# Optimization experiments

Measured on AMD Instinct MI355X. Metric: run time of the kernel, lower is better.

The kernel has to match this reference:

```python
import jax, jax.numpy as jnp
import numpy as np
import math

V, D, H, L, DFF = 32000, 1024, 16, 4, 4096
B, T_TGT, T_SRC = 4, 512, 512


def setup_inputs() -> dict:
    key = jax.random.key(0)
    ks = iter(jax.random.split(key, 64))
    s = 0.02
    inp = {
        'tgt': jax.random.randint(next(ks), (B, T_TGT), 0, V, dtype=jnp.int32),
        'encoder_output': jax.random.normal(next(ks), (B, T_SRC, D), jnp.float32),
        'tgt_mask': jnp.tril(jnp.ones((T_TGT, T_TGT), jnp.int32)),
        'emb': jax.random.normal(next(ks), (V, D)) * s,
        'Wout': jax.random.normal(next(ks), (D, V)) * s,
        'bout': jnp.zeros((V,)),
    }
    for pfx in ('s', 'c'):  # self / cross attention
        for nm in ('q', 'k', 'v', 'o'):
            inp[f'W{nm}_{pfx}'] = jax.random.normal(next(ks), (L, D, D)) * s
            inp[f'b{nm}_{pfx}'] = jnp.zeros((L, D))
    inp['W1'] = jax.random.normal(next(ks), (L, D, DFF)) * s
    inp['b1'] = jnp.zeros((L, DFF))
    inp['W2'] = jax.random.normal(next(ks), (L, DFF, D)) * s
    inp['b2'] = jnp.zeros((L, D))
    for i in (1, 2, 3):
        inp[f'ln{i}_g'] = jnp.ones((L, D))
        inp[f'ln{i}_b'] = jnp.zeros((L, D))
    return inp


def _layernorm(x, g, b, eps=1e-5):
    m = x.mean(-1, keepdims=True)
    v = ((x - m) ** 2).mean(-1, keepdims=True)
    return g * (x - m) * jax.lax.rsqrt(v + eps) + b


def _mha(xq, xkv, Wq, bq, Wk, bk, Wv, bv, Wo, bo, mask):
    Bq, Tq, Dm = xq.shape
    dk = Dm // H
    q = (xq @ Wq + bq).reshape(Bq, Tq, H, dk).transpose(0, 2, 1, 3)   # bhqd
    k = (xkv @ Wk + bk).reshape(Bq, -1, H, dk).transpose(0, 2, 1, 3)  # bhkd
    v = (xkv @ Wv + bv).reshape(Bq, -1, H, dk).transpose(0, 2, 1, 3)
    scores = jnp.einsum('bhqd,bhkd->bhqk', q, k) / math.sqrt(dk)
    if mask is not None:
        scores = jnp.where(mask[None, None] == 0, -1e9, scores)
    w = jax.nn.softmax(scores, axis=-1)                               # dropout: eval mode
    o = jnp.einsum('bhqk,bhkd->bhqd', w, v).transpose(0, 2, 1, 3).reshape(Bq, Tq, Dm)
    return o @ Wo + bo, w


def _pos_encoding(T, Dm):
    pos = jnp.arange(T, dtype=jnp.float32)[:, None]
    div = jnp.exp(jnp.arange(0, Dm, 2, dtype=jnp.float32) * (-math.log(10000.0) / Dm))
    pe = jnp.zeros((T, Dm))
    pe = pe.at[:, 0::2].set(jnp.sin(pos * div))
    pe = pe.at[:, 1::2].set(jnp.cos(pos * div))
    return pe


def reference(tgt, encoder_output, tgt_mask, emb, Wout, bout,
              Wq_s, bq_s, Wk_s, bk_s, Wv_s, bv_s, Wo_s, bo_s,
              Wq_c, bq_c, Wk_c, bk_c, Wv_c, bv_c, Wo_c, bo_c,
              W1, b1, W2, b2, ln1_g, ln1_b, ln2_g, ln2_b, ln3_g, ln3_b):
    x = emb[tgt] * math.sqrt(D) + _pos_encoding(tgt.shape[1], D)[None]
    self_ws, cross_ws = [], []
    for i in range(L):
        a1, sw = _mha(x, x, Wq_s[i], bq_s[i], Wk_s[i], bk_s[i], Wv_s[i], bv_s[i],
                      Wo_s[i], bo_s[i], tgt_mask)
        x = _layernorm(x + a1, ln1_g[i], ln1_b[i])
        a2, cw = _mha(x, encoder_output, Wq_c[i], bq_c[i], Wk_c[i], bk_c[i],
                      Wv_c[i], bv_c[i], Wo_c[i], bo_c[i], None)
        x = _layernorm(x + a2, ln2_g[i], ln2_b[i])
        ffn = jax.nn.relu(x @ W1[i] + b1[i]) @ W2[i] + b2[i]
        x = _layernorm(x + ffn, ln3_g[i], ln3_b[i])
        self_ws.append(sw)
        cross_ws.append(cw)
    logits = x @ Wout + bout
    return logits, jnp.stack(self_ws), jnp.stack(cross_ws)
```

## Files before the change

### kernel.cpp

```cpp
#include <hip/hip_runtime.h>


typedef unsigned short u16;
typedef __bf16 v8bf __attribute__((ext_vector_type(8)));
typedef float v4f __attribute__((ext_vector_type(4)));

namespace {
constexpr int kB = 4, kT = 512, kD = 1024, kH = 16, kDK = 64, kF = 4096, kV = 32000, kL = 4;
constexpr int kM = kB * kT;
constexpr long kTD = (long)kT * kD;
constexpr long kTT = (long)kT * kT;
constexpr long kHTT = (long)kH * kTT;
constexpr long kBHTT = (long)kB * kHTT;
constexpr long kLOG = (long)kM * kV;
constexpr long kPART = (long)kM * kD;
}

__device__ __forceinline__ u16 f2bf(float f) {
  union { float f; unsigned u; } v; v.f = f;
  unsigned r = v.u + 0x7FFFu + ((v.u >> 16) & 1u);
  return (u16)(r >> 16);
}
__device__ __forceinline__ float bf2f(u16 h) {
  union { unsigned u; float f; } v; v.u = ((unsigned)h) << 16;
  return v.f;
}

typedef __attribute__((address_space(3))) void lds_void;
typedef const __attribute__((address_space(1))) void glob_void;
__device__ __forceinline__ void gl2lds16(const void* g, void* l) {
  __builtin_amdgcn_global_load_lds((glob_void*)g, (lds_void*)l, 16, 0, 0);
}

template <int BM, int BN, int OUTBF>
__global__ __launch_bounds__(256)
void gemm_bf(const u16* __restrict__ A0, const u16* __restrict__ B0,
             const float* __restrict__ bias, void* __restrict__ Cv,
             const int K, const int lda, const int ldb, const int ldc,
             const int nH, const long sAb, const long sAh,
             const long sBb, const long sBh, const long sCb, const long sCh,
             const float scale, const int relu) {
  static_assert(BM % 32 == 0 && BN % 32 == 0, "tiles");
  __shared__ u16 As[BM][64];
  __shared__ u16 Bs[BN][64];
  const int tid = threadIdx.x;
  const int lane = tid & 63;
  const int w = tid >> 6;
  const int z = blockIdx.z;
  const int zb = z / nH, zh = z - zb * nH;
  const u16* A = A0 + zb * sAb + zh * sAh + (long)blockIdx.y * BM * lda;
  const u16* B = B0 + zb * sBb + zh * sBh + (long)blockIdx.x * BN * ldb;
  const long offC = zb * sCb + zh * sCh;
  const int wm = w >> 1, wn = w & 1;
  constexpr int FM = BM / 32, FN = BN / 32;
  v4f acc[FM][FN];
  const v4f zero = {0.f, 0.f, 0.f, 0.f};
#pragma unroll
  for (int i = 0; i < FM; ++i)
#pragma unroll
    for (int j = 0; j < FN; ++j) acc[i][j] = zero;
  const int l15 = lane & 15, lk = lane >> 4;
  const int lr8 = lane >> 3;
  const int lc8 = (lane & 7) * 8;

  for (int k0 = 0; k0 < K; k0 += 64) {
    __syncthreads();
#pragma unroll
    for (int s = 0; s < BM / 32; ++s)
      gl2lds16(A + (long)(w * (BM / 4) + s * 8 + lr8) * lda + k0 + lc8,
               &As[w * (BM / 4) + s * 8][0]);
#pragma unroll
    for (int s = 0; s < BN / 32; ++s)
      gl2lds16(B + (long)(w * (BN / 4) + s * 8 + lr8) * ldb + k0 + lc8,
               &Bs[w * (BN / 4) + s * 8][0]);
    __syncthreads();
#pragma unroll
    for (int t = 0; t < 2; ++t) {
      v8bf af[FM], bfr[FN];
#pragma unroll
      for (int i = 0; i < FM; ++i)
        af[i] = *(const v8bf*)&As[wm * (BM / 2) + i * 16 + l15][t * 32 + lk * 8];
#pragma unroll
      for (int j = 0; j < FN; ++j)
        bfr[j] = *(const v8bf*)&Bs[wn * (BN / 2) + j * 16 + l15][t * 32 + lk * 8];
#pragma unroll
      for (int i = 0; i < FM; ++i)
#pragma unroll
        for (int j = 0; j < FN; ++j)
          acc[i][j] = __builtin_amdgcn_mfma_f32_16x16x32_bf16(af[i], bfr[j], acc[i][j], 0, 0, 0);
    }
  }

  const long m0 = (long)blockIdx.y * BM + wm * (BM / 2);
  const int n0 = blockIdx.x * BN + wn * (BN / 2);
#pragma unroll
  for (int j = 0; j < FN; ++j) {
    const int col = n0 + j * 16 + l15;
    const float bv = (bias && zb == 0) ? bias[col] : 0.0f;
#pragma unroll
    for (int i = 0; i < FM; ++i) {
      const long row = m0 + i * 16 + lk * 4;
#pragma unroll
      for (int r = 0; r < 4; ++r) {
        float v = acc[i][j][r] * scale + bv;
        if (relu) v = fmaxf(v, 0.0f);
        const long idx = offC + (row + r) * ldc + col;
        if (OUTBF) ((u16*)Cv)[idx] = f2bf(v);
        else       ((float*)Cv)[idx] = v;
      }
    }
  }
}

template <int CAUSAL>
__global__ __launch_bounds__(512)
void attn_scores(const u16* __restrict__ Qb, const u16* __restrict__ Kb,
                 float* __restrict__ wout, u16* __restrict__ pb) {
  __shared__ u16 Qs[128][64];
  __shared__ u16 Ks[512][64];
  __shared__ float redM[128][4];
  __shared__ float redS[128][4];
  const int tid = threadIdx.x, lane = tid & 63, w = tid >> 6;
  const int wm = w >> 2, wn = w & 3;
  const int l15 = lane & 15, lk = lane >> 4;
  const int lr8 = lane >> 3, lc8 = (lane & 7) * 8;
  const int bx = blockIdx.x;
  const int z = blockIdx.y, zb = z >> 4, zh = z & 15;
  const u16* Q = Qb + (long)zb * 512 * 3072 + zh * 64 + (long)bx * 128 * 3072;
  const u16* Kp = Kb + (long)zb * 512 * 3072 + zh * 64;
  const long obase = (long)zb * kHTT + (long)zh * kTT;

#pragma unroll
  for (int s = 0; s < 2; ++s)
    gl2lds16(Q + (long)(w * 16 + s * 8 + lr8) * 3072 + lc8, &Qs[w * 16 + s * 8][0]);
#pragma unroll
  for (int s = 0; s < 8; ++s) {
    const int r0 = w * 64 + s * 8;
    if (!CAUSAL || r0 <= bx * 128 + 127)
      gl2lds16(Kp + (long)(r0 + lr8) * 3072 + lc8, &Ks[r0][0]);
  }
  __syncthreads();

  v4f acc[4][8];
  const v4f zero = {0.f, 0.f, 0.f, 0.f};
#pragma unroll
  for (int i = 0; i < 4; ++i)
#pragma unroll
    for (int j = 0; j < 8; ++j) acc[i][j] = zero;

#pragma unroll
  for (int t = 0; t < 2; ++t) {
    v8bf aq[4], bk[8];
#pragma unroll
    for (int i = 0; i < 4; ++i)
      aq[i] = *(const v8bf*)&Qs[wm * 64 + i * 16 + l15][t * 32 + lk * 8];
#pragma unroll
    for (int j = 0; j < 8; ++j)
      bk[j] = *(const v8bf*)&Ks[wn * 128 + j * 16 + l15][t * 32 + lk * 8];
#pragma unroll
    for (int i = 0; i < 4; ++i)
#pragma unroll
      for (int j = 0; j < 8; ++j) {
        if (!(CAUSAL && wn * 128 + j * 16 > bx * 128 + wm * 64 + i * 16 + 15))
          acc[i][j] = __builtin_amdgcn_mfma_f32_16x16x32_bf16(aq[i], bk[j], acc[i][j], 0, 0, 0);
      }
  }

  float gmax[4][4];
#pragma unroll
  for (int i = 0; i < 4; ++i)
#pragma unroll
    for (int r = 0; r < 4; ++r) {
      const int q = bx * 128 + wm * 64 + i * 16 + lk * 4 + r;
      float m = -3.0e38f;
#pragma unroll
      for (int j = 0; j < 8; ++j) {
        const int col = wn * 128 + j * 16 + l15;
        if (!CAUSAL || col <= q) m = fmaxf(m, acc[i][j][r] * 0.125f);
      }
#pragma unroll
      for (int off = 1; off < 16; off <<= 1) m = fmaxf(m, __shfl_xor(m, off));
      if (l15 == 0) redM[wm * 64 + i * 16 + lk * 4 + r][wn] = m;
    }
  __syncthreads();
#pragma unroll
  for (int i = 0; i < 4; ++i)
#pragma unroll
    for (int r = 0; r < 4; ++r) {
      v4f mv = *(const v4f*)&redM[wm * 64 + i * 16 + lk * 4 + r][0];
      gmax[i][r] = fmaxf(fmaxf(mv[0], mv[1]), fmaxf(mv[2], mv[3]));
    }
#pragma unroll
  for (int i = 0; i < 4; ++i)
#pragma unroll
    for (int r = 0; r < 4; ++r) {
      const int q = bx * 128 + wm * 64 + i * 16 + lk * 4 + r;
      float s = 0.0f;
#pragma unroll
      for (int j = 0; j < 8; ++j) {
        const int col = wn * 128 + j * 16 + l15;
        float e = (!CAUSAL || col <= q) ? __expf(acc[i][j][r] * 0.125f - gmax[i][r]) : 0.0f;
        acc[i][j][r] = e;
        s += e;
      }
#pragma unroll
      for (int off = 1; off < 16; off <<= 1) s += __shfl_xor(s, off);
      if (l15 == 0) redS[wm * 64 + i * 16 + lk * 4 + r][wn] = s;
    }
  __syncthreads();
#pragma unroll
  for (int i = 0; i < 4; ++i)
#pragma unroll
    for (int r = 0; r < 4; ++r) {
      v4f sv = *(const v4f*)&redS[wm * 64 + i * 16 + lk * 4 + r][0];
      const float inv = 1.0f / (sv[0] + sv[1] + sv[2] + sv[3]);
      const int q = bx * 128 + wm * 64 + i * 16 + lk * 4 + r;
      const long rowoff = obase + (long)q * 512;
#pragma unroll
      for (int j = 0; j < 8; ++j) {
        const int col = wn * 128 + j * 16 + l15;
        const float v = acc[i][j][r] * inv;
        wout[rowoff + col] = v;
        pb[rowoff + col] = f2bf(v);
      }
    }
}

struct TPtrs { const float* in[8]; u16* out[8]; };

__global__ void transpose_wt_v2(TPtrs ps, int K, int N) {
  __shared__ float tile[32][33];
  const float* in = ps.in[blockIdx.z];
  u16* o = ps.out[blockIdx.z];
  const int n0 = blockIdx.x * 32, k0 = blockIdx.y * 32;
  const int tx = threadIdx.x, ty = threadIdx.y;
#pragma unroll
  for (int i = 0; i < 4; ++i)
    tile[ty + 8 * i][tx] = in[(long)(k0 + ty + 8 * i) * N + n0 + tx];
  __syncthreads();
#pragma unroll
  for (int i = 0; i < 4; ++i)
    o[(long)(n0 + ty + 8 * i) * K + k0 + tx] = f2bf(tile[tx][ty + 8 * i]);
}

__global__ void concat_bias(float* __restrict__ dst, const float* __restrict__ s0,
                            const float* __restrict__ s1, const float* __restrict__ s2,
                            const int nsrc) {
  const int idx = blockIdx.x * 256 + threadIdx.x;
  const int per = nsrc << 10;
  const int l = idx / per, rem = idx - l * per, s = rem >> 10, j = rem & 1023;
  const float* src = (s == 0) ? s0 : (s == 1 ? s1 : s2);
  dst[idx] = src[l * 1024 + j];
}

__global__ void cvt_bf16_v2(const float* __restrict__ in, u16* __restrict__ o) {
  const long i = ((long)blockIdx.x * 256 + threadIdx.x) * 4;
  float4 v = *(const float4*)(in + i);
  u16 h[4] = {f2bf(v.x), f2bf(v.y), f2bf(v.z), f2bf(v.w)};
  *(uint2*)(o + i) = *(const uint2*)h;
}

__global__ void embed_v2(const int* __restrict__ tgt, const float* __restrict__ emb,
                         float* __restrict__ x, u16* __restrict__ xb) {
  const int row = blockIdx.x;
  const int t = row & (kT - 1);
  const int tok = tgt[row];
  const int c = threadIdx.x * 4;
  float4 e = *(const float4*)(emb + (long)tok * kD + c);
  const float nl = -9.210340371976184f / (float)kD;
  const float a0 = (float)t * expf((float)c * nl);
  const float a1 = (float)t * expf((float)(c + 2) * nl);
  float4 o;
  o.x = e.x * 32.0f + sinf(a0);
  o.y = e.y * 32.0f + cosf(a0);
  o.z = e.z * 32.0f + sinf(a1);
  o.w = e.w * 32.0f + cosf(a1);
  *(float4*)(x + (long)row * kD + c) = o;
  u16 h[4] = {f2bf(o.x), f2bf(o.y), f2bf(o.z), f2bf(o.w)};
  *(uint2*)(xb + (long)row * kD + c) = *(const uint2*)h;
}

__global__ void transpose_v_v2(const u16* __restrict__ Sqkv, u16* __restrict__ vt) {
  __shared__ u16 tile[32][33];
  const int z = blockIdx.z, b = z >> 4, h = z & 15;
  const int t0 = blockIdx.x * 32, d0 = blockIdx.y * 32;
  const int tx = threadIdx.x, ty = threadIdx.y;
  const u16* in = Sqkv + (long)b * kT * 3072 + 2048 + h * kDK;
#pragma unroll
  for (int i = 0; i < 4; ++i)
    tile[ty + 8 * i][tx] = in[(long)(t0 + ty + 8 * i) * 3072 + d0 + tx];
  __syncthreads();
  u16* o = vt + (long)z * kDK * kT;
#pragma unroll
  for (int i = 0; i < 4; ++i)
    o[(long)(d0 + ty + 8 * i) * kT + t0 + tx] = tile[tx][ty + 8 * i];
}

__global__ void add_ln_v3(float* __restrict__ x, u16* __restrict__ xb,
                          const float* __restrict__ res, const int nres,
                          const float* __restrict__ g, const float* __restrict__ b) {
  const int row = blockIdx.x;
  const int c = threadIdx.x * 4;
  float4 xv = *(const float4*)(x + (long)row * kD + c);
  float v0 = xv.x, v1 = xv.y, v2 = xv.z, v3 = xv.w;
  for (int p = 0; p < nres; ++p) {
    float4 rv = *(const float4*)(res + p * kPART + (long)row * kD + c);
    v0 += rv.x; v1 += rv.y; v2 += rv.z; v3 += rv.w;
  }
  float s = v0 + v1 + v2 + v3;
  float ss = v0 * v0 + v1 * v1 + v2 * v2 + v3 * v3;
#pragma unroll
  for (int o = 32; o > 0; o >>= 1) { s += __shfl_xor(s, o); ss += __shfl_xor(ss, o); }
  __shared__ float red[4][2];
  const int wv = threadIdx.x >> 6;
  if ((threadIdx.x & 63) == 0) { red[wv][0] = s; red[wv][1] = ss; }
  __syncthreads();
  s  = red[0][0] + red[1][0] + red[2][0] + red[3][0];
  ss = red[0][1] + red[1][1] + red[2][1] + red[3][1];
  const float mean = s * (1.0f / kD);
  const float var = ss * (1.0f / kD) - mean * mean;
  const float rs = rsqrtf(var + 1e-5f);
  float4 gv = *(const float4*)(g + c);
  float4 bv = *(const float4*)(b + c);
  float4 o;
  o.x = gv.x * (v0 - mean) * rs + bv.x;
  o.y = gv.y * (v1 - mean) * rs + bv.y;
  o.z = gv.z * (v2 - mean) * rs + bv.z;
  o.w = gv.w * (v3 - mean) * rs + bv.w;
  *(float4*)(x + (long)row * kD + c) = o;
  u16 h[4] = {f2bf(o.x), f2bf(o.y), f2bf(o.z), f2bf(o.w)};
  *(uint2*)(xb + (long)row * kD + c) = *(const uint2*)h;
}

template <int BM, int BN, typename TA, typename TB, int BKN>
__global__ __launch_bounds__(256)
void gemm_kernel(const void* __restrict__ Av, const void* __restrict__ Bv,
                 const float* __restrict__ bias, float* __restrict__ Cv,
                 const int K, const int lda, const int ldb, const int ldc,
                 const int nH, const long sAb, const long sAh,
                 const long sBb, const long sBh, const long sCb, const long sCh,
                 const float scale, const int relu) {
  constexpr int LP = 40;
  __shared__ u16 As[BM][LP];
  __shared__ u16 Bs[BN][LP];
  const int tid = threadIdx.x;
  const int z = blockIdx.z;
  const int zb = z / nH, zh = z - zb * nH;
  const TA* A = (const TA*)Av + zb * sAb + zh * sAh + (long)blockIdx.y * BM * lda;
  const TB* Bp;
  if constexpr (BKN)
    Bp = (const TB*)Bv + zb * sBb + zh * sBh + (long)blockIdx.x * BN;
  else
    Bp = (const TB*)Bv + zb * sBb + zh * sBh + (long)blockIdx.x * BN * ldb;
  const long offC = zb * sCb + zh * sCh;
  const int lane = tid & 63;
  const int wm = (tid >> 7) & 1, wn = (tid >> 6) & 1;
  constexpr int FM = BM / 32, FN = BN / 32;
  v4f acc[FM][FN];
  const v4f zero = {0.f, 0.f, 0.f, 0.f};
#pragma unroll
  for (int i = 0; i < FM; ++i)
#pragma unroll
    for (int j = 0; j < FN; ++j) acc[i][j] = zero;
  const int l15 = lane & 15, lk = lane >> 4;

  for (int k0 = 0; k0 < K; k0 += 32) {
    __syncthreads();
    if constexpr (sizeof(TA) == 4) {
      const int r = tid >> 3, c = (tid & 7) * 4;
#pragma unroll
      for (int rr = 0; rr < BM; rr += 32) {
        float4 vv = *(const float4*)((const float*)A + (long)(rr + r) * lda + k0 + c);
        unsigned lo = (unsigned)f2bf(vv.x) | ((unsigned)f2bf(vv.y) << 16);
        unsigned hi = (unsigned)f2bf(vv.z) | ((unsigned)f2bf(vv.w) << 16);
        *(uint2*)&As[rr + r][c] = make_uint2(lo, hi);
      }
    } else {
      const int r = tid >> 2, c = (tid & 3) * 8;
#pragma unroll
      for (int rr = 0; rr < BM; rr += 64) {
        uint4 vv = *(const uint4*)((const u16*)A + (long)(rr + r) * lda + k0 + c);
        *(uint4*)&As[rr + r][c] = vv;
      }
    }
    if constexpr (BKN) {
      const int r = tid >> 3, c = (tid & 7) * 4;
#pragma unroll
      for (int nn = 0; nn < BN; nn += 32) {
        float4 vv = *(const float4*)((const float*)Bp + (long)(k0 + r) * ldb + nn + c);
        Bs[nn + c + 0][r] = f2bf(vv.x);
        Bs[nn + c + 1][r] = f2bf(vv.y);
        Bs[nn + c + 2][r] = f2bf(vv.z);
        Bs[nn + c + 3][r] = f2bf(vv.w);
      }
    } else if constexpr (sizeof(TB) == 4) {
      const int r = tid >> 3, c = (tid & 7) * 4;
#pragma unroll
      for (int rr = 0; rr < BN; rr += 32) {
        float4 vv = *(const float4*)((const float*)Bp + (long)(rr + r) * ldb + k0 + c);
        unsigned lo = (unsigned)f2bf(vv.x) | ((unsigned)f2bf(vv.y) << 16);
        unsigned hi = (unsigned)f2bf(vv.z) | ((unsigned)f2bf(vv.w) << 16);
        *(uint2*)&Bs[rr + r][c] = make_uint2(lo, hi);
      }
    } else {
      const int r = tid >> 2, c = (tid & 3) * 8;
#pragma unroll
      for (int rr = 0; rr < BN; rr += 64) {
        uint4 vv = *(const uint4*)((const u16*)Bp + (long)(rr + r) * ldb + k0 + c);
        *(uint4*)&Bs[rr + r][c] = vv;
      }
    }
    __syncthreads();
    v8bf af[FM], bfr[FN];
#pragma unroll
    for (int i = 0; i < FM; ++i)
      af[i] = *(const v8bf*)&As[wm * (BM / 2) + i * 16 + l15][lk * 8];
#pragma unroll
    for (int j = 0; j < FN; ++j)
      bfr[j] = *(const v8bf*)&Bs[wn * (BN / 2) + j * 16 + l15][lk * 8];
#pragma unroll
    for (int i = 0; i < FM; ++i)
#pragma unroll
      for (int j = 0; j < FN; ++j)
        acc[i][j] = __builtin_amdgcn_mfma_f32_16x16x32_bf16(af[i], bfr[j], acc[i][j], 0, 0, 0);
  }

  const long m0 = (long)blockIdx.y * BM + wm * (BM / 2);
  const int n0 = blockIdx.x * BN + wn * (BN / 2);
#pragma unroll
  for (int j = 0; j < FN; ++j) {
    const int col = n0 + j * 16 + l15;
    const float bv = bias ? bias[col] : 0.0f;
#pragma unroll
    for (int i = 0; i < FM; ++i) {
      const long row = m0 + i * 16 + lk * 4;
#pragma unroll
      for (int r = 0; r < 4; ++r) {
        float v = acc[i][j][r] * scale + bv;
        if (relu) v = fmaxf(v, 0.0f);
        Cv[offC + (row + r) * ldc + col] = v;
      }
    }
  }
}

__global__ void embed_kernel(const int* __restrict__ tgt, const float* __restrict__ emb,
                             float* __restrict__ x) {
  const int row = blockIdx.x;
  const int t = row & (kT - 1);
  const int tok = tgt[row];
  const int c = threadIdx.x * 4;
  float4 e = *(const float4*)(emb + (long)tok * kD + c);
  const float nl = -9.210340371976184f / (float)kD;
  const float a0 = (float)t * expf((float)c * nl);
  const float a1 = (float)t * expf((float)(c + 2) * nl);
  float4 o;
  o.x = e.x * 32.0f + sinf(a0);
  o.y = e.y * 32.0f + cosf(a0);
  o.z = e.z * 32.0f + sinf(a1);
  o.w = e.w * 32.0f + cosf(a1);
  *(float4*)(x + (long)row * kD + c) = o;
}

__global__ void transpose_v_kernel(const float* __restrict__ v, u16* __restrict__ vt) {
  __shared__ float tile[32][33];
  const int z = blockIdx.z;
  const int b = z >> 4, h = z & 15;
  const int t0 = blockIdx.x * 32, d0 = blockIdx.y * 32;
  const int tx = threadIdx.x, ty = threadIdx.y;
  const float* in = v + (long)b * kTD + (long)h * kDK;
#pragma unroll
  for (int i = 0; i < 4; ++i)
    tile[ty + 8 * i][tx] = in[(long)(t0 + ty + 8 * i) * kD + d0 + tx];
  __syncthreads();
  u16* o = vt + (long)z * kDK * kT;
#pragma unroll
  for (int i = 0; i < 4; ++i)
    o[(long)(d0 + ty + 8 * i) * kT + t0 + tx] = f2bf(tile[tx][ty + 8 * i]);
}

__global__ void softmax_kernel(float* __restrict__ w, const int causal) {
  const int rowg = blockIdx.x * 4 + (threadIdx.x >> 6);
  const int lane = threadIdx.x & 63;
  const int q = rowg & (kT - 1);
  float* p = w + (long)rowg * kT + lane * 8;
  float4 v0 = *(const float4*)p;
  float4 v1 = *(const float4*)(p + 4);
  float f[8] = {v0.x, v0.y, v0.z, v0.w, v1.x, v1.y, v1.z, v1.w};
  const int base = lane * 8;
  float mx = -3.0e38f;
#pragma unroll
  for (int j = 0; j < 8; ++j)
    if (!causal || base + j <= q) mx = fmaxf(mx, f[j]);
#pragma unroll
  for (int o = 32; o > 0; o >>= 1) mx = fmaxf(mx, __shfl_xor(mx, o));
  float s = 0.0f;
#pragma unroll
  for (int j = 0; j < 8; ++j) {
    float e = (!causal || base + j <= q) ? __expf(f[j] - mx) : 0.0f;
    f[j] = e; s += e;
  }
#pragma unroll
  for (int o = 32; o > 0; o >>= 1) s += __shfl_xor(s, o);
  const float inv = 1.0f / s;
  float4 o0 = {f[0] * inv, f[1] * inv, f[2] * inv, f[3] * inv};
  float4 o1 = {f[4] * inv, f[5] * inv, f[6] * inv, f[7] * inv};
  *(float4*)p = o0;
  *(float4*)(p + 4) = o1;
}

__global__ void add_ln_kernel(float* __restrict__ x, const float* __restrict__ res,
                              const float* __restrict__ g, const float* __restrict__ b) {
  const int row = blockIdx.x;
  const int c = threadIdx.x * 4;
  float4 xv = *(const float4*)(x + (long)row * kD + c);
  float4 rv = *(const float4*)(res + (long)row * kD + c);
  const float v0 = xv.x + rv.x, v1 = xv.y + rv.y, v2 = xv.z + rv.z, v3 = xv.w + rv.w;
  float s = v0 + v1 + v2 + v3;
  float ss = v0 * v0 + v1 * v1 + v2 * v2 + v3 * v3;
#pragma unroll
  for (int o = 32; o > 0; o >>= 1) { s += __shfl_xor(s, o); ss += __shfl_xor(ss, o); }
  __shared__ float red[4][2];
  const int wv = threadIdx.x >> 6;
  if ((threadIdx.x & 63) == 0) { red[wv][0] = s; red[wv][1] = ss; }
  __syncthreads();
  s  = red[0][0] + red[1][0] + red[2][0] + red[3][0];
  ss = red[0][1] + red[1][1] + red[2][1] + red[3][1];
  const float mean = s * (1.0f / kD);
  const float var = ss * (1.0f / kD) - mean * mean;
  const float rs = rsqrtf(var + 1e-5f);
  float4 gv = *(const float4*)(g + c);
  float4 bv = *(const float4*)(b + c);
  float4 o;
  o.x = gv.x * (v0 - mean) * rs + bv.x;
  o.y = gv.y * (v1 - mean) * rs + bv.y;
  o.z = gv.z * (v2 - mean) * rs + bv.z;
  o.w = gv.w * (v3 - mean) * rs + bv.w;
  *(float4*)(x + (long)row * kD + c) = o;
}

extern "C" void kernel_launch(void* const* d_in, const int* in_sizes, int n_in,
                              void* d_out, int out_size, void* d_ws, size_t ws_size,
                              hipStream_t stream) {
  const int*   tgt  = (const int*)d_in[0];
  const float* enc  = (const float*)d_in[1];
  const float* emb  = (const float*)d_in[3];
  const float* Wout = (const float*)d_in[4];
  const float* bout = (const float*)d_in[5];
  const float* Wq_s = (const float*)d_in[6];
  const float* bq_s = (const float*)d_in[7];
  const float* Wk_s = (const float*)d_in[8];
  const float* bk_s = (const float*)d_in[9];
  const float* Wv_s = (const float*)d_in[10];
  const float* bv_s = (const float*)d_in[11];
  const float* Wo_s = (const float*)d_in[12];
  const float* bo_s = (const float*)d_in[13];
  const float* Wq_c = (const float*)d_in[14];
  const float* bq_c = (const float*)d_in[15];
  const float* Wk_c = (const float*)d_in[16];
  const float* bk_c = (const float*)d_in[17];
  const float* Wv_c = (const float*)d_in[18];
  const float* bv_c = (const float*)d_in[19];
  const float* Wo_c = (const float*)d_in[20];
  const float* bo_c = (const float*)d_in[21];
  const float* W1   = (const float*)d_in[22];
  const float* b1   = (const float*)d_in[23];
  const float* W2   = (const float*)d_in[24];
  const float* b2   = (const float*)d_in[25];
  const float* ln1g = (const float*)d_in[26];
  const float* ln1b = (const float*)d_in[27];
  const float* ln2g = (const float*)d_in[28];
  const float* ln2b = (const float*)d_in[29];
  const float* ln3g = (const float*)d_in[30];
  const float* ln3b = (const float*)d_in[31];

  float* out = (float*)d_out;
  const long DD = (long)kD * kD;
  const dim3 blk256(256), blkT(32, 8);

  if (ws_size >= (320ll << 20)) {
    char* ws = (char*)d_ws;
    float* x     = (float*)ws;
    u16* xb      = (u16*)(ws + (8l << 20));
    u16* encb    = (u16*)(ws + (12l << 20));
    u16* Sqkv    = (u16*)(ws + (16l << 20));
    u16* vt      = (u16*)(ws + (28l << 20));
    u16* S3b     = (u16*)(ws + (32l << 20));
    u16* Hb      = (u16*)(ws + (36l << 20));
    float* Spart = (float*)(ws + (52l << 20));
    u16* Pb      = (u16*)(ws + (84l << 20));
    u16* wbase   = (u16*)(ws + (116l << 20));
    u16* woutT   = (u16*)(ws + (244l << 20));
    float* bqkvS = (float*)(ws + (308l << 20));
    float* bkvC  = (float*)(ws + (308l << 20) + (64l << 10));
    const long WLAY = (32l << 20) / 2;

    for (int i = 0; i < kL; ++i) {
      u16* wqkvS = wbase + i * WLAY;
      u16* woS   = wqkvS + 3072 * 1024;
      u16* wqC   = woS + 1024 * 1024;
      u16* wkvC  = wqC + 1024 * 1024;
      u16* woC   = wkvC + 2048 * 1024;
      u16* w1t   = woC + 1024 * 1024;
      u16* w2t   = w1t + (long)4096 * 1024;
      TPtrs p{};
      p.in[0] = Wq_s + i * DD; p.out[0] = wqkvS;
      p.in[1] = Wk_s + i * DD; p.out[1] = wqkvS + 1024 * 1024;
      p.in[2] = Wv_s + i * DD; p.out[2] = wqkvS + 2048 * 1024;
      p.in[3] = Wo_s + i * DD; p.out[3] = woS;
      p.in[4] = Wq_c + i * DD; p.out[4] = wqC;
      p.in[5] = Wk_c + i * DD; p.out[5] = wkvC;
      p.in[6] = Wv_c + i * DD; p.out[6] = wkvC + 1024 * 1024;
      p.in[7] = Wo_c + i * DD; p.out[7] = woC;
      transpose_wt_v2<<<dim3(32, 32, 8), blkT, 0, stream>>>(p, 1024, 1024);
      TPtrs p1{}; p1.in[0] = W1 + (long)i * kD * kF; p1.out[0] = w1t;
      transpose_wt_v2<<<dim3(128, 32, 1), blkT, 0, stream>>>(p1, 1024, 4096);
      TPtrs p2{}; p2.in[0] = W2 + (long)i * kF * kD; p2.out[0] = w2t;
      transpose_wt_v2<<<dim3(32, 128, 1), blkT, 0, stream>>>(p2, 4096, 1024);
    }
    TPtrs po{}; po.in[0] = Wout; po.out[0] = woutT;
    transpose_wt_v2<<<dim3(1000, 32, 1), blkT, 0, stream>>>(po, 1024, 32000);
    concat_bias<<<dim3(48), blk256, 0, stream>>>(bqkvS, bq_s, bk_s, bv_s, 3);
    concat_bias<<<dim3(32), blk256, 0, stream>>>(bkvC, bk_c, bv_c, nullptr, 2);
    cvt_bf16_v2<<<dim3(2048), blk256, 0, stream>>>(enc, encb);
    embed_v2<<<dim3(kM), blk256, 0, stream>>>(tgt, emb, x, xb);

    for (int i = 0; i < kL; ++i) {
      u16* wqkvS = wbase + i * WLAY;
      u16* woS   = wqkvS + 3072 * 1024;
      u16* wqC   = woS + 1024 * 1024;
      u16* wkvC  = wqC + 1024 * 1024;
      u16* woC   = wkvC + 2048 * 1024;
      u16* w1t   = woC + 1024 * 1024;
      u16* w2t   = w1t + (long)4096 * 1024;
      float* wSelf  = out + kLOG + (long)i * kBHTT;
      float* wCross = out + kLOG + (long)kL * kBHTT + (long)i * kBHTT;

      gemm_bf<128, 128, 1><<<dim3(24, 16, 1), blk256, 0, stream>>>(
          xb, wqkvS, bqkvS + i * 3072, Sqkv, 1024, 1024, 1024, 3072,
          1, 0, 0, 0, 0, 0, 0, 1.0f, 0);
      transpose_v_v2<<<dim3(16, 2, 64), blkT, 0, stream>>>(Sqkv, vt);
      attn_scores<1><<<dim3(4, 64), dim3(512), 0, stream>>>(Sqkv, Sqkv + 1024, wSelf, Pb);
      gemm_bf<128, 64, 1><<<dim3(1, 4, 64), blk256, 0, stream>>>(
          Pb, vt, nullptr, S3b, 512, 512, 512, 1024,
          16, kHTT, kTT, 16l * 32768, 32768, 512l * 1024, 64, 1.0f, 0);
      gemm_bf<128, 128, 0><<<dim3(8, 16, 2), blk256, 0, stream>>>(
          S3b, woS, bo_s + (long)i * kD, Spart, 512, 1024, 1024, 1024,
          1, 512, 0, 512, 0, kPART, 0, 1.0f, 0);
      add_ln_v3<<<dim3(kM), blk256, 0, stream>>>(x, xb, Spart, 2,
          ln1g + (long)i * kD, ln1b + (long)i * kD);

      gemm_bf<128, 128, 1><<<dim3(8, 16, 1), blk256, 0, stream>>>(
          xb, wqC, bq_c + (long)i * kD, Sqkv, 1024, 1024, 1024, 3072,
          1, 0, 0, 0, 0, 0, 0, 1.0f, 0);
      gemm_bf<128, 128, 1><<<dim3(16, 16, 1), blk256, 0, stream>>>(
          encb, wkvC, bkvC + i * 2048, Sqkv + 1024, 1024, 1024, 1024, 3072,
          1, 0, 0, 0, 0, 0, 0, 1.0f, 0);
      transpose_v_v2<<<dim3(16, 2, 64), blkT, 0, stream>>>(Sqkv, vt);
      attn_scores<0><<<dim3(4, 64), dim3(512), 0, stream>>>(Sqkv, Sqkv + 1024, wCross, Pb);
      gemm_bf<128, 64, 1><<<dim3(1, 4, 64), blk256, 0, stream>>>(
          Pb, vt, nullptr, S3b, 512, 512, 512, 1024,
          16, kHTT, kTT, 16l * 32768, 32768, 512l * 1024, 64, 1.0f, 0);
      gemm_bf<128, 128, 0><<<dim3(8, 16, 2), blk256, 0, stream>>>(
          S3b, woC, bo_c + (long)i * kD, Spart, 512, 1024, 1024, 1024,
          1, 512, 0, 512, 0, kPART, 0, 1.0f, 0);
      add_ln_v3<<<dim3(kM), blk256, 0, stream>>>(x, xb, Spart, 2,
          ln2g + (long)i * kD, ln2b + (long)i * kD);

      gemm_bf<128, 128, 1><<<dim3(32, 16, 1), blk256, 0, stream>>>(
          xb, w1t, b1 + (long)i * kF, Hb, 1024, 1024, 1024, 4096,
          1, 0, 0, 0, 0, 0, 0, 1.0f, 1);
      gemm_bf<128, 128, 0><<<dim3(8, 16, 4), blk256, 0, stream>>>(
          Hb, w2t, b2 + (long)i * kD, Spart, 1024, 4096, 4096, 1024,
          1, 1024, 0, 1024, 0, kPART, 0, 1.0f, 0);
      add_ln_v3<<<dim3(kM), blk256, 0, stream>>>(x, xb, Spart, 4,
          ln3g + (long)i * kD, ln3b + (long)i * kD);
    }

    gemm_bf<128, 128, 0><<<dim3(250, 16, 1), blk256, 0, stream>>>(
        xb, woutT, bout, out, 1024, 1024, 1024, 32000,
        1, 0, 0, 0, 0, 0, 0, 1.0f, 0);
    return;
  }

  float* x = (float*)d_ws;
  char* sc = (char*)d_out;
  float* S0 = (float*)sc;
  float* S1 = (float*)(sc + (8l  << 20));
  float* S2 = (float*)(sc + (16l << 20));
  float* S3 = (float*)(sc + (24l << 20));
  float* S4 = (float*)(sc + (32l << 20));
  u16*   vt = (u16*)  (sc + (40l << 20));

  embed_kernel<<<dim3(kM), blk256, 0, stream>>>(tgt, emb, x);
  auto wgemm = [&](const float* A, const float* W, const float* bias, float* C) {
    gemm_kernel<128, 128, float, float, 1><<<dim3(kD / 128, kM / 128, 1), blk256, 0, stream>>>(
        A, W, bias, C, kD, kD, kD, kD, 1, 0, 0, 0, 0, 0, 0, 1.0f, 0);
  };
  for (int i = 0; i < kL; ++i) {
    const long wOff = (long)i * DD;
    float* wSelf  = out + kLOG + (long)i * kBHTT;
    float* wCross = out + kLOG + (long)kL * kBHTT + (long)i * kBHTT;
    wgemm(x, Wq_s + wOff, bq_s + (long)i * kD, S0);
    wgemm(x, Wk_s + wOff, bk_s + (long)i * kD, S1);
    wgemm(x, Wv_s + wOff, bv_s + (long)i * kD, S2);
    transpose_v_kernel<<<dim3(16, 2, 64), blkT, 0, stream>>>(S2, vt);
    gemm_kernel<128, 128, float, float, 0><<<dim3(4, 4, 64), blk256, 0, stream>>>(
        S0, S1, nullptr, wSelf, kDK, kD, kD, kT,
        kH, kTD, (long)kDK, kTD, (long)kDK, kHTT, kTT, 0.125f, 0);
    softmax_kernel<<<dim3(kB * kH * kT / 4), blk256, 0, stream>>>(wSelf, 1);
    gemm_kernel<128, 64, float, u16, 0><<<dim3(1, 4, 64), blk256, 0, stream>>>(
        wSelf, vt, nullptr, S3, kT, kT, kT, kD,
        kH, kHTT, kTT, (long)kH * kDK * kT, (long)kDK * kT, kTD, (long)kDK, 1.0f, 0);
    wgemm(S3, Wo_s + wOff, bo_s + (long)i * kD, S0);
    add_ln_kernel<<<dim3(kM), blk256, 0, stream>>>(x, S0, ln1g + (long)i * kD, ln1b + (long)i * kD);
    wgemm(x,   Wq_c + wOff, bq_c + (long)i * kD, S0);
    wgemm(enc, Wk_c + wOff, bk_c + (long)i * kD, S1);
    wgemm(enc, Wv_c + wOff, bv_c + (long)i * kD, S2);
    transpose_v_kernel<<<dim3(16, 2, 64), blkT, 0, stream>>>(S2, vt);
    gemm_kernel<128, 128, float, float, 0><<<dim3(4, 4, 64), blk256, 0, stream>>>(
        S0, S1, nullptr, wCross, kDK, kD, kD, kT,
        kH, kTD, (long)kDK, kTD, (long)kDK, kHTT, kTT, 0.125f, 0);
    softmax_kernel<<<dim3(kB * kH * kT / 4), blk256, 0, stream>>>(wCross, 0);
    gemm_kernel<128, 64, float, u16, 0><<<dim3(1, 4, 64), blk256, 0, stream>>>(
        wCross, vt, nullptr, S3, kT, kT, kT, kD,
        kH, kHTT, kTT, (long)kH * kDK * kT, (long)kDK * kT, kTD, (long)kDK, 1.0f, 0);
    wgemm(S3, Wo_c + wOff, bo_c + (long)i * kD, S0);
    add_ln_kernel<<<dim3(kM), blk256, 0, stream>>>(x, S0, ln2g + (long)i * kD, ln2b + (long)i * kD);
    gemm_kernel<128, 128, float, float, 1><<<dim3(kF / 128, kM / 128, 1), blk256, 0, stream>>>(
        x, W1 + (long)i * kD * kF, b1 + (long)i * kF, S0, kD, kD, kF, kF,
        1, 0, 0, 0, 0, 0, 0, 1.0f, 1);
    gemm_kernel<128, 128, float, float, 1><<<dim3(kD / 128, kM / 128, 1), blk256, 0, stream>>>(
        S0, W2 + (long)i * kF * kD, b2 + (long)i * kD, S4, kF, kF, kD, kD,
        1, 0, 0, 0, 0, 0, 0, 1.0f, 0);
    add_ln_kernel<<<dim3(kM), blk256, 0, stream>>>(x, S4, ln3g + (long)i * kD, ln3b + (long)i * kD);
  }
  gemm_kernel<128, 128, float, float, 1><<<dim3(kV / 128, kM / 128, 1), blk256, 0, stream>>>(
      x, Wout, bout, out, kD, kD, kV, kV,
      1, 0, 0, 0, 0, 0, 0, 1.0f, 0);
}
```

Before: 1.685 ms.

## Fuse attention PV into score kernel, swizzle LDS, merge cross-attn QKV GEMMs

Attention now computes P·V inside the softmax kernel, using LDS staging, instead of writing a bf16 probability matrix and running a separate batched GEMM. The V-transpose kernel is removed: the QKV GEMM epilogue writes transposed V directly. LDS tiles in the GEMM and attention kernels use an XOR swizzle to reduce bank conflicts. Cross-attention Q and KV projections are merged into one launch via the z dimension, and FFN2 split-K drops from 4 to 2 partials. In exchange, the epilogue does extra scattered stores and the fused kernel loops serially over key chunks.

```diff
diff --git a/kernel.cpp b/kernel.cpp
--- a/kernel.cpp
+++ b/kernel.cpp
@@ -32,14 +32,15 @@
   __builtin_amdgcn_global_load_lds((glob_void*)g, (lds_void*)l, 16, 0, 0);
 }
 
-template <int BM, int BN, int OUTBF>
+template <int BM, int BN, int OUTBF, int VTR>
 __global__ __launch_bounds__(256)
 void gemm_bf(const u16* __restrict__ A0, const u16* __restrict__ B0,
              const float* __restrict__ bias, void* __restrict__ Cv,
+             u16* __restrict__ vtw,
              const int K, const int lda, const int ldb, const int ldc,
              const int nH, const long sAb, const long sAh,
              const long sBb, const long sBh, const long sCb, const long sCh,
-             const float scale, const int relu) {
+             const float scale, const int relu, const int bstride) {
   static_assert(BM % 32 == 0 && BN % 32 == 0, "tiles");
   __shared__ u16 As[BM][64];
   __shared__ u16 Bs[BN][64];
@@ -61,28 +62,30 @@
     for (int j = 0; j < FN; ++j) acc[i][j] = zero;
   const int l15 = lane & 15, lk = lane >> 4;
   const int lr8 = lane >> 3;
-  const int lc8 = (lane & 7) * 8;
+  const int swz = ((lane & 7) ^ lr8) * 8;
+  const int l7 = l15 & 7;
 
   for (int k0 = 0; k0 < K; k0 += 64) {
     __syncthreads();
 #pragma unroll
     for (int s = 0; s < BM / 32; ++s)
-      gl2lds16(A + (long)(w * (BM / 4) + s * 8 + lr8) * lda + k0 + lc8,
+      gl2lds16(A + (long)(w * (BM / 4) + s * 8 + lr8) * lda + k0 + swz,
                &As[w * (BM / 4) + s * 8][0]);
 #pragma unroll
     for (int s = 0; s < BN / 32; ++s)
-      gl2lds16(B + (long)(w * (BN / 4) + s * 8 + lr8) * ldb + k0 + lc8,
+      gl2lds16(B + (long)(w * (BN / 4) + s * 8 + lr8) * ldb + k0 + swz,
                &Bs[w * (BN / 4) + s * 8][0]);
     __syncthreads();
 #pragma unroll
     for (int t = 0; t < 2; ++t) {
+      const int c0 = t * 4;
       v8bf af[FM], bfr[FN];
 #pragma unroll
       for (int i = 0; i < FM; ++i)
-        af[i] = *(const v8bf*)&As[wm * (BM / 2) + i * 16 + l15][t * 32 + lk * 8];
+        af[i] = *(const v8bf*)&As[wm * (BM / 2) + i * 16 + l15][((c0 + lk) ^ l7) * 8];
 #pragma unroll
       for (int j = 0; j < FN; ++j)
-        bfr[j] = *(const v8bf*)&Bs[wn * (BN / 2) + j * 16 + l15][t * 32 + lk * 8];
+        bfr[j] = *(const v8bf*)&Bs[wn * (BN / 2) + j * 16 + l15][((c0 + lk) ^ l7) * 8];
 #pragma unroll
       for (int i = 0; i < FM; ++i)
 #pragma unroll
@@ -96,7 +99,7 @@
 #pragma unroll
   for (int j = 0; j < FN; ++j) {
     const int col = n0 + j * 16 + l15;
-    const float bv = (bias && zb == 0) ? bias[col] : 0.0f;
+    const float bv = (bias && zb == 0) ? bias[zh * bstride + col] : 0.0f;
 #pragma unroll
     for (int i = 0; i < FM; ++i) {
       const long row = m0 + i * 16 + lk * 4;
@@ -107,6 +110,14 @@
         const long idx = offC + (row + r) * ldc + col;
         if (OUTBF) ((u16*)Cv)[idx] = f2bf(v);
         else       ((float*)Cv)[idx] = v;
+        if (VTR) {
+          const int colS = (int)(offC % 3072) + col;
+          if (colS >= 2048) {
+            const int hh = (colS - 2048) >> 6, dd = (colS - 2048) & 63;
+            const int rowg = (int)(row + r);
+            vtw[((long)((rowg >> 9) * 16 + hh)) * 32768 + dd * 512 + (rowg & 511)] = f2bf(v);
+          }
+        }
       }
     }
   }
@@ -114,30 +125,37 @@
 
 template <int CAUSAL>
 __global__ __launch_bounds__(512)
-void attn_scores(const u16* __restrict__ Qb, const u16* __restrict__ Kb,
-                 float* __restrict__ wout, u16* __restrict__ pb) {
-  __shared__ u16 Qs[128][64];
-  __shared__ u16 Ks[512][64];
+void attn_fused(const u16* __restrict__ Qb, const u16* __restrict__ Kb,
+                const u16* __restrict__ vtp, float* __restrict__ wout,
+                u16* __restrict__ oout) {
+  __shared__ __align__(16) char lds[81920];
+  u16 (*Qs)[64] = (u16 (*)[64])lds;
+  u16 (*Ks)[64] = (u16 (*)[64])(lds + 16384);
+  u16 (*Pl)[136] = (u16 (*)[136])lds;
+  u16 (*Vt)[136] = (u16 (*)[136])(lds + 34816);
   __shared__ float redM[128][4];
   __shared__ float redS[128][4];
   const int tid = threadIdx.x, lane = tid & 63, w = tid >> 6;
   const int wm = w >> 2, wn = w & 3;
   const int l15 = lane & 15, lk = lane >> 4;
-  const int lr8 = lane >> 3, lc8 = (lane & 7) * 8;
+  const int lr8 = lane >> 3;
+  const int swz = ((lane & 7) ^ lr8) * 8;
+  const int l7 = l15 & 7;
   const int bx = blockIdx.x;
   const int z = blockIdx.y, zb = z >> 4, zh = z & 15;
   const u16* Q = Qb + (long)zb * 512 * 3072 + zh * 64 + (long)bx * 128 * 3072;
   const u16* Kp = Kb + (long)zb * 512 * 3072 + zh * 64;
+  const u16* vtz = vtp + (long)((zb << 4) + zh) * 32768;
   const long obase = (long)zb * kHTT + (long)zh * kTT;
 
 #pragma unroll
   for (int s = 0; s < 2; ++s)
-    gl2lds16(Q + (long)(w * 16 + s * 8 + lr8) * 3072 + lc8, &Qs[w * 16 + s * 8][0]);
+    gl2lds16(Q + (long)(w * 16 + s * 8 + lr8) * 3072 + swz, &Qs[w * 16 + s * 8][0]);
 #pragma unroll
   for (int s = 0; s < 8; ++s) {
     const int r0 = w * 64 + s * 8;
     if (!CAUSAL || r0 <= bx * 128 + 127)
-      gl2lds16(Kp + (long)(r0 + lr8) * 3072 + lc8, &Ks[r0][0]);
+      gl2lds16(Kp + (long)(r0 + lr8) * 3072 + swz, &Ks[r0][0]);
   }
   __syncthreads();
 
@@ -150,20 +168,20 @@
 
 #pragma unroll
   for (int t = 0; t < 2; ++t) {
+    const int c0 = t * 4;
     v8bf aq[4], bk[8];
 #pragma unroll
     for (int i = 0; i < 4; ++i)
-      aq[i] = *(const v8bf*)&Qs[wm * 64 + i * 16 + l15][t * 32 + lk * 8];
+      aq[i] = *(const v8bf*)&Qs[wm * 64 + i * 16 + l15][((c0 + lk) ^ l7) * 8];
 #pragma unroll
     for (int j = 0; j < 8; ++j)
-      bk[j] = *(const v8bf*)&Ks[wn * 128 + j * 16 + l15][t * 32 + lk * 8];
+      bk[j] = *(const v8bf*)&Ks[wn * 128 + j * 16 + l15][((c0 + lk) ^ l7) * 8];
 #pragma unroll
     for (int i = 0; i < 4; ++i)
 #pragma unroll
-      for (int j = 0; j < 8; ++j) {
+      for (int j = 0; j < 8; ++j)
         if (!(CAUSAL && wn * 128 + j * 16 > bx * 128 + wm * 64 + i * 16 + 15))
           acc[i][j] = __builtin_amdgcn_mfma_f32_16x16x32_bf16(aq[i], bk[j], acc[i][j], 0, 0, 0);
-      }
   }
 
   float gmax[4][4];
@@ -220,9 +238,52 @@
       for (int j = 0; j < 8; ++j) {
         const int col = wn * 128 + j * 16 + l15;
         const float v = acc[i][j][r] * inv;
+        acc[i][j][r] = v;
         wout[rowoff + col] = v;
-        pb[rowoff + col] = f2bf(v);
-      }
+      }
+    }
+
+  v4f acco[4];
+#pragma unroll
+  for (int i = 0; i < 4; ++i) acco[i] = zero;
+  const int kcMax = CAUSAL ? bx : 3;
+  for (int kc = 0; kc <= kcMax; ++kc) {
+    __syncthreads();
+    if (wn == kc) {
+#pragma unroll
+      for (int i = 0; i < 4; ++i)
+#pragma unroll
+        for (int j = 0; j < 8; ++j) {
+          const int colk = j * 16 + l15;
+#pragma unroll
+          for (int r = 0; r < 4; ++r)
+            Pl[wm * 64 + i * 16 + lk * 4 + r][colk] = f2bf(acc[i][j][r]);
+        }
+    }
+#pragma unroll
+    for (int s = 0; s < 2; ++s) {
+      const int c = tid * 2 + s;
+      const int d = c >> 4, off = (c & 15) * 8;
+      uint4 vv = *(const uint4*)(vtz + (long)d * 512 + kc * 128 + off);
+      *(uint4*)&Vt[d][off] = vv;
+    }
+    __syncthreads();
+#pragma unroll
+    for (int t = 0; t < 4; ++t) {
+      v8bf bv = *(const v8bf*)&Vt[wn * 16 + l15][t * 32 + lk * 8];
+#pragma unroll
+      for (int i = 0; i < 4; ++i) {
+        v8bf ap = *(const v8bf*)&Pl[wm * 64 + i * 16 + l15][t * 32 + lk * 8];
+        acco[i] = __builtin_amdgcn_mfma_f32_16x16x32_bf16(ap, bv, acco[i], 0, 0, 0);
+      }
+    }
+  }
+#pragma unroll
+  for (int i = 0; i < 4; ++i)
+#pragma unroll
+    for (int r = 0; r < 4; ++r) {
+      const int row = bx * 128 + wm * 64 + i * 16 + lk * 4 + r;
+      oout[(long)(zb * 512 + row) * 1024 + zh * 64 + wn * 16 + l15] = f2bf(acco[i][r]);
     }
 }
 
@@ -253,11 +314,13 @@
   dst[idx] = src[l * 1024 + j];
 }
 
-__global__ void cvt_bf16_v2(const float* __restrict__ in, u16* __restrict__ o) {
+__global__ void cvt_bf16_v3(const float* __restrict__ in, u16* __restrict__ o1,
+                            u16* __restrict__ o2) {
   const long i = ((long)blockIdx.x * 256 + threadIdx.x) * 4;
   float4 v = *(const float4*)(in + i);
   u16 h[4] = {f2bf(v.x), f2bf(v.y), f2bf(v.z), f2bf(v.w)};
-  *(uint2*)(o + i) = *(const uint2*)h;
+  *(uint2*)(o1 + i) = *(const uint2*)h;
+  *(uint2*)(o2 + i) = *(const uint2*)h;
 }
 
 __global__ void embed_v2(const int* __restrict__ tgt, const float* __restrict__ emb,
@@ -278,22 +341,6 @@
   *(float4*)(x + (long)row * kD + c) = o;
   u16 h[4] = {f2bf(o.x), f2bf(o.y), f2bf(o.z), f2bf(o.w)};
   *(uint2*)(xb + (long)row * kD + c) = *(const uint2*)h;
-}
-
-__global__ void transpose_v_v2(const u16* __restrict__ Sqkv, u16* __restrict__ vt) {
-  __shared__ u16 tile[32][33];
-  const int z = blockIdx.z, b = z >> 4, h = z & 15;
-  const int t0 = blockIdx.x * 32, d0 = blockIdx.y * 32;
-  const int tx = threadIdx.x, ty = threadIdx.y;
-  const u16* in = Sqkv + (long)b * kT * 3072 + 2048 + h * kDK;
-#pragma unroll
-  for (int i = 0; i < 4; ++i)
-    tile[ty + 8 * i][tx] = in[(long)(t0 + ty + 8 * i) * 3072 + d0 + tx];
-  __syncthreads();
-  u16* o = vt + (long)z * kDK * kT;
-#pragma unroll
-  for (int i = 0; i < 4; ++i)
-    o[(long)(d0 + ty + 8 * i) * kT + t0 + tx] = tile[tx][ty + 8 * i];
 }
 
 __global__ void add_ln_v3(float* __restrict__ x, u16* __restrict__ xb,
@@ -578,29 +625,28 @@
   const long DD = (long)kD * kD;
   const dim3 blk256(256), blkT(32, 8);
 
-  if (ws_size >= (320ll << 20)) {
+  if (ws_size >= (272ll << 20)) {
     char* ws = (char*)d_ws;
     float* x     = (float*)ws;
     u16* xb      = (u16*)(ws + (8l << 20));
     u16* encb    = (u16*)(ws + (12l << 20));
-    u16* Sqkv    = (u16*)(ws + (16l << 20));
-    u16* vt      = (u16*)(ws + (28l << 20));
-    u16* S3b     = (u16*)(ws + (32l << 20));
-    u16* Hb      = (u16*)(ws + (36l << 20));
-    float* Spart = (float*)(ws + (52l << 20));
-    u16* Pb      = (u16*)(ws + (84l << 20));
-    u16* wbase   = (u16*)(ws + (116l << 20));
-    u16* woutT   = (u16*)(ws + (244l << 20));
-    float* bqkvS = (float*)(ws + (308l << 20));
-    float* bkvC  = (float*)(ws + (308l << 20) + (64l << 10));
-    const long WLAY = (32l << 20) / 2;
+    u16* encb2   = (u16*)(ws + (16l << 20));
+    u16* Sqkv    = (u16*)(ws + (20l << 20));
+    u16* vt      = (u16*)(ws + (32l << 20));
+    u16* S3b     = (u16*)(ws + (36l << 20));
+    u16* Hb      = (u16*)(ws + (40l << 20));
+    float* Spart = (float*)(ws + (56l << 20));
+    u16* wbase   = (u16*)(ws + (72l << 20));
+    u16* woutT   = (u16*)(ws + (200l << 20));
+    float* bqkvS = (float*)(ws + (263l << 20));
+    float* bqkvC = (float*)(ws + (263l << 20) + (64l << 10));
+    const long WLAY = 16l * 1024 * 1024;
 
     for (int i = 0; i < kL; ++i) {
       u16* wqkvS = wbase + i * WLAY;
       u16* woS   = wqkvS + 3072 * 1024;
-      u16* wqC   = woS + 1024 * 1024;
-      u16* wkvC  = wqC + 1024 * 1024;
-      u16* woC   = wkvC + 2048 * 1024;
+      u16* wqkvC = woS + 1024 * 1024;
+      u16* woC   = wqkvC + 3072 * 1024;
       u16* w1t   = woC + 1024 * 1024;
       u16* w2t   = w1t + (long)4096 * 1024;
       TPtrs p{};
@@ -608,9 +654,9 @@
       p.in[1] = Wk_s + i * DD; p.out[1] = wqkvS + 1024 * 1024;
       p.in[2] = Wv_s + i * DD; p.out[2] = wqkvS + 2048 * 1024;
       p.in[3] = Wo_s + i * DD; p.out[3] = woS;
-      p.in[4] = Wq_c + i * DD; p.out[4] = wqC;
-      p.in[5] = Wk_c + i * DD; p.out[5] = wkvC;
-      p.in[6] = Wv_c + i * DD; p.out[6] = wkvC + 1024 * 1024;
+      p.in[4] = Wq_c + i * DD; p.out[4] = wqkvC;
+      p.in[5] = Wk_c + i * DD; p.out[5] = wqkvC + 1024 * 1024;
+      p.in[6] = Wv_c + i * DD; p.out[6] = wqkvC + 2048 * 1024;
       p.in[7] = Wo_c + i * DD; p.out[7] = woC;
       transpose_wt_v2<<<dim3(32, 32, 8), blkT, 0, stream>>>(p, 1024, 1024);
       TPtrs p1{}; p1.in[0] = W1 + (long)i * kD * kF; p1.out[0] = w1t;
@@ -621,65 +667,53 @@
     TPtrs po{}; po.in[0] = Wout; po.out[0] = woutT;
     transpose_wt_v2<<<dim3(1000, 32, 1), blkT, 0, stream>>>(po, 1024, 32000);
     concat_bias<<<dim3(48), blk256, 0, stream>>>(bqkvS, bq_s, bk_s, bv_s, 3);
-    concat_bias<<<dim3(32), blk256, 0, stream>>>(bkvC, bk_c, bv_c, nullptr, 2);
-    cvt_bf16_v2<<<dim3(2048), blk256, 0, stream>>>(enc, encb);
+    concat_bias<<<dim3(48), blk256, 0, stream>>>(bqkvC, bq_c, bk_c, bv_c, 3);
+    cvt_bf16_v3<<<dim3(2048), blk256, 0, stream>>>(enc, encb, encb2);
     embed_v2<<<dim3(kM), blk256, 0, stream>>>(tgt, emb, x, xb);
 
     for (int i = 0; i < kL; ++i) {
       u16* wqkvS = wbase + i * WLAY;
       u16* woS   = wqkvS + 3072 * 1024;
-      u16* wqC   = woS + 1024 * 1024;
-      u16* wkvC  = wqC + 1024 * 1024;
-      u16* woC   = wkvC + 2048 * 1024;
+      u16* wqkvC = woS + 1024 * 1024;
+      u16* woC   = wqkvC + 3072 * 1024;
       u16* w1t   = woC + 1024 * 1024;
       u16* w2t   = w1t + (long)4096 * 1024;
       float* wSelf  = out + kLOG + (long)i * kBHTT;
       float* wCross = out + kLOG + (long)kL * kBHTT + (long)i * kBHTT;
 
-      gemm_bf<128, 128, 1><<<dim3(24, 16, 1), blk256, 0, stream>>>(
-          xb, wqkvS, bqkvS + i * 3072, Sqkv, 1024, 1024, 1024, 3072,
-          1, 0, 0, 0, 0, 0, 0, 1.0f, 0);
-      transpose_v_v2<<<dim3(16, 2, 64), blkT, 0, stream>>>(Sqkv, vt);
-      attn_scores<1><<<dim3(4, 64), dim3(512), 0, stream>>>(Sqkv, Sqkv + 1024, wSelf, Pb);
-      gemm_bf<128, 64, 1><<<dim3(1, 4, 64), blk256, 0, stream>>>(
-          Pb, vt, nullptr, S3b, 512, 512, 512, 1024,
-          16, kHTT, kTT, 16l * 32768, 32768, 512l * 1024, 64, 1.0f, 0);
-      gemm_bf<128, 128, 0><<<dim3(8, 16, 2), blk256, 0, stream>>>(
-          S3b, woS, bo_s + (long)i * kD, Spart, 512, 1024, 1024, 1024,
-          1, 512, 0, 512, 0, kPART, 0, 1.0f, 0);
+      gemm_bf<128, 128, 1, 1><<<dim3(24, 16, 1), blk256, 0, stream>>>(
+          xb, wqkvS, bqkvS + i * 3072, Sqkv, vt, 1024, 1024, 1024, 3072,
+          1, 0, 0, 0, 0, 0, 0, 1.0f, 0, 0);
+      attn_fused<1><<<dim3(4, 64), dim3(512), 0, stream>>>(Sqkv, Sqkv + 1024, vt, wSelf, S3b);
+      gemm_bf<128, 128, 0, 0><<<dim3(8, 16, 2), blk256, 0, stream>>>(
+          S3b, woS, bo_s + (long)i * kD, Spart, nullptr, 512, 1024, 1024, 1024,
+          1, 512, 0, 512, 0, kPART, 0, 1.0f, 0, 0);
       add_ln_v3<<<dim3(kM), blk256, 0, stream>>>(x, xb, Spart, 2,
           ln1g + (long)i * kD, ln1b + (long)i * kD);
 
-      gemm_bf<128, 128, 1><<<dim3(8, 16, 1), blk256, 0, stream>>>(
-          xb, wqC, bq_c + (long)i * kD, Sqkv, 1024, 1024, 1024, 3072,
-          1, 0, 0, 0, 0, 0, 0, 1.0f, 0);
-      gemm_bf<128, 128, 1><<<dim3(16, 16, 1), blk256, 0, stream>>>(
-          encb, wkvC, bkvC + i * 2048, Sqkv + 1024, 1024, 1024, 1024, 3072,
-          1, 0, 0, 0, 0, 0, 0, 1.0f, 0);
-      transpose_v_v2<<<dim3(16, 2, 64), blkT, 0, stream>>>(Sqkv, vt);
-      attn_scores<0><<<dim3(4, 64), dim3(512), 0, stream>>>(Sqkv, Sqkv + 1024, wCross, Pb);
-      gemm_bf<128, 64, 1><<<dim3(1, 4, 64), blk256, 0, stream>>>(
-          Pb, vt, nullptr, S3b, 512, 512, 512, 1024,
-          16, kHTT, kTT, 16l * 32768, 32768, 512l * 1024, 64, 1.0f, 0);
-      gemm_bf<128, 128, 0><<<dim3(8, 16, 2), blk256, 0, stream>>>(
-          S3b, woC, bo_c + (long)i * kD, Spart, 512, 1024, 1024, 1024,
-          1, 512, 0, 512, 0, kPART, 0, 1.0f, 0);
+      gemm_bf<128, 128, 1, 1><<<dim3(8, 16, 3), blk256, 0, stream>>>(
+          xb, wqkvC, bqkvC + i * 3072, Sqkv, vt, 1024, 1024, 1024, 3072,
+          3, 0, (long)2048 * 1024, 0, (long)1024 * 1024, 0, 1024, 1.0f, 0, 1024);
+      attn_fused<0><<<dim3(4, 64), dim3(512), 0, stream>>>(Sqkv, Sqkv + 1024, vt, wCross, S3b);
+      gemm_bf<128, 128, 0, 0><<<dim3(8, 16, 2), blk256, 0, stream>>>(
+          S3b, woC, bo_c + (long)i * kD, Spart, nullptr, 512, 1024, 1024, 1024,
+          1, 512, 0, 512, 0, kPART, 0, 1.0f, 0, 0);
       add_ln_v3<<<dim3(kM), blk256, 0, stream>>>(x, xb, Spart, 2,
           ln2g + (long)i * kD, ln2b + (long)i * kD);
 
-      gemm_bf<128, 128, 1><<<dim3(32, 16, 1), blk256, 0, stream>>>(
-          xb, w1t, b1 + (long)i * kF, Hb, 1024, 1024, 1024, 4096,
-          1, 0, 0, 0, 0, 0, 0, 1.0f, 1);
-      gemm_bf<128, 128, 0><<<dim3(8, 16, 4), blk256, 0, stream>>>(
-          Hb, w2t, b2 + (long)i * kD, Spart, 1024, 4096, 4096, 1024,
-          1, 1024, 0, 1024, 0, kPART, 0, 1.0f, 0);
-      add_ln_v3<<<dim3(kM), blk256, 0, stream>>>(x, xb, Spart, 4,
+      gemm_bf<128, 128, 1, 0><<<dim3(32, 16, 1), blk256, 0, stream>>>(
+          xb, w1t, b1 + (long)i * kF, Hb, nullptr, 1024, 1024, 1024, 4096,
+          1, 0, 0, 0, 0, 0, 0, 1.0f, 1, 0);
+      gemm_bf<128, 128, 0, 0><<<dim3(8, 16, 2), blk256, 0, stream>>>(
+          Hb, w2t, b2 + (long)i * kD, Spart, nullptr, 2048, 4096, 4096, 1024,
+          1, 2048, 0, 2048, 0, kPART, 0, 1.0f, 0, 0);
+      add_ln_v3<<<dim3(kM), blk256, 0, stream>>>(x, xb, Spart, 2,
           ln3g + (long)i * kD, ln3b + (long)i * kD);
     }
 
-    gemm_bf<128, 128, 0><<<dim3(250, 16, 1), blk256, 0, stream>>>(
-        xb, woutT, bout, out, 1024, 1024, 1024, 32000,
-        1, 0, 0, 0, 0, 0, 0, 1.0f, 0);
+    gemm_bf<128, 128, 0, 0><<<dim3(250, 16, 1), blk256, 0, stream>>>(
+        xb, woutT, bout, out, nullptr, 1024, 1024, 1024, 32000,
+        1, 0, 0, 0, 0, 0, 0, 1.0f, 0, 0);
     return;
   }
 
```

New measurement: 1.585 ms. 1.06x faster.
